# Performance work log

Hardware: AMD Instinct MI355X
Metric: run time of the kernel (lower is better)

Reference implementation:

```python
import jax, jax.numpy as jnp
import numpy as np

B, T, P = 256, 64, 10          # games, vote steps, players (cell_num)
E = 64                          # embedding_size -> node feat dim 2E=128
D = 2 * E
HID = 64                        # lstm_hidden_size
EPS = 1e-8


def setup_inputs() -> dict:
    key = jax.random.key(0)
    ks = jax.random.split(key, 12)
    s = 0.1  # param init scale
    return {
        "x": jax.random.normal(ks[0], (B, T, P, D), jnp.float32),
        "A_pos": jax.random.uniform(ks[1], (B, T, P, P), jnp.float32),
        "A_neg": jax.random.uniform(ks[2], (B, T, P, P), jnp.float32),
        "W_pos_base": s * jax.random.normal(ks[3], (2 * D, 32), jnp.float32),
        "b_pos_base": jnp.zeros((32,), jnp.float32),
        "W_neg_base": s * jax.random.normal(ks[4], (2 * D, 32), jnp.float32),
        "b_neg_base": jnp.zeros((32,), jnp.float32),
        "W_pos_deep": s * jax.random.normal(ks[5], (2, 7 * 32, 32), jnp.float32),
        "b_pos_deep": jnp.zeros((2, 32), jnp.float32),
        "W_neg_deep": s * jax.random.normal(ks[6], (2, 7 * 32, 32), jnp.float32),
        "b_neg_deep": jnp.zeros((2, 32), jnp.float32),
        "W_ih": s * jax.random.normal(ks[7], (P, 4 * HID, 2 * 32), jnp.float32),
        "W_hh": s * jax.random.normal(ks[8], (P, 4 * HID, HID), jnp.float32),
        "b_ih": jnp.zeros((P, 4 * HID), jnp.float32),
        "b_hh": jnp.zeros((P, 4 * HID), jnp.float32),
    }


def _sgcn(x, A_pos, A_neg, W_pos_base, b_pos_base, W_neg_base, b_neg_base,
          W_pos_deep, b_pos_deep, W_neg_deep, b_neg_deep):
    # mean aggregation: row-normalized signed adjacencies, shape [B,T,P,P]
    An_p = A_pos / (jnp.sum(A_pos, axis=-1, keepdims=True) + EPS)
    An_n = A_neg / (jnp.sum(A_neg, axis=-1, keepdims=True) + EPS)
    agg = lambda A, h: jnp.einsum('btij,btjd->btid', A, h)
    # base aggregators: cat([mean_neighbors, self]) @ W  -> [B,T,P,32]
    h_pos = jnp.tanh(jnp.concatenate([agg(An_p, x), x], -1) @ W_pos_base + b_pos_base)
    h_neg = jnp.tanh(jnp.concatenate([agg(An_n, x), x], -1) @ W_neg_base + b_neg_base)
    # two deep layers per sign: 7 concatenated 32-d blocks
    for i in range(2):
        ap_p, ap_n = agg(An_p, h_pos), agg(An_p, h_neg)
        an_p, an_n = agg(An_n, h_pos), agg(An_n, h_neg)
        common = [ap_p, ap_n, an_p, an_n, h_pos, h_neg]
        new_pos = jnp.tanh(jnp.concatenate(common + [h_pos], -1) @ W_pos_deep[i] + b_pos_deep[i])
        new_neg = jnp.tanh(jnp.concatenate(common + [h_neg], -1) @ W_neg_deep[i] + b_neg_deep[i])
        h_pos, h_neg = new_pos, new_neg
    return jnp.concatenate([h_pos, h_neg], -1)  # [B,T,P,64]


def _lstm(z, W_ih, W_hh, b_ih, b_hh):
    # per-player LSTMCell recurrence over vote steps (torch.nn.LSTMCell math)
    zT = jnp.moveaxis(z, 1, 0)  # [T,B,P,64]
    bias = b_ih + b_hh          # [P,4H]

    def step(carry, z_t):
        h, c = carry  # [B,P,H]
        gates = (jnp.einsum('bpi,pgi->bpg', z_t, W_ih)
                 + jnp.einsum('bph,pgh->bpg', h, W_hh) + bias)
        i, f, g, o = jnp.split(gates, 4, axis=-1)
        c_new = jax.nn.sigmoid(f) * c + jax.nn.sigmoid(i) * jnp.tanh(g)
        h_new = jax.nn.sigmoid(o) * jnp.tanh(c_new)
        return (h_new, c_new), h_new

    init = (jnp.zeros((z.shape[0], P, HID), z.dtype),
            jnp.zeros((z.shape[0], P, HID), z.dtype))
    _, hs = jax.lax.scan(step, init, zT)
    return jnp.moveaxis(hs, 0, 1)  # [B,T,P,H]


def reference(x, A_pos, A_neg, W_pos_base, b_pos_base, W_neg_base, b_neg_base,
              W_pos_deep, b_pos_deep, W_neg_deep, b_neg_deep,
              W_ih, W_hh, b_ih, b_hh):
    z = _sgcn(x, A_pos, A_neg, W_pos_base, b_pos_base, W_neg_base, b_neg_base,
              W_pos_deep, b_pos_deep, W_neg_deep, b_neg_deep)
    return _lstm(z, W_ih, W_hh, b_ih, b_hh)
```

## Files before the change

### kernel.cpp

```cpp
#include <hip/hip_runtime.h>
#include <stdint.h>

#define Bg 256
#define Tg 64
#define Pg 10
#define NG 8
#define GL 4

typedef _Float16 half2v __attribute__((ext_vector_type(2)));
typedef _Float16 f16x8 __attribute__((ext_vector_type(8)));
typedef float f32x4v __attribute__((ext_vector_type(4)));

__device__ __forceinline__ float dot2(uint32_t a, uint32_t b, float c) {
#if __has_builtin(__builtin_amdgcn_fdot2)
    return __builtin_amdgcn_fdot2(__builtin_bit_cast(half2v, a),
                                  __builtin_bit_cast(half2v, b), c, false);
#else
    float d;
    asm("v_dot2_f32_f16 %0, %1, %2, %3"
        : "=v"(d) : "v"(a), "v"(b), "v"(c));
    return d;
#endif
}

__device__ __forceinline__ uint32_t pkh2(float lo, float hi) {
    half2v h; h.x = (_Float16)lo; h.y = (_Float16)hi;
    return __builtin_bit_cast(uint32_t, h);
}
__device__ __forceinline__ uint16_t f2h(float f) {
    _Float16 h = (_Float16)f;
    return __builtin_bit_cast(uint16_t, h);
}
__device__ __forceinline__ float h2f(uint16_t u) {
    _Float16 h = __builtin_bit_cast(_Float16, u);
    return (float)h;
}
__device__ __forceinline__ float2 up2(uint32_t u) {
    half2v h = __builtin_bit_cast(half2v, u);
    return make_float2((float)h.x, (float)h.y);
}
__device__ __forceinline__ float sigmoidf_(float x) {
    return 1.0f / (1.0f + __expf(-x));
}
__device__ __forceinline__ float fast_tanh(float x) {
    float e = __expf(2.0f * x);
    return (e - 1.0f) / (e + 1.0f);
}

__global__ __launch_bounds__(512) void sgcn_kernel(
    const float* __restrict__ x,
    const float* __restrict__ A_pos,
    const float* __restrict__ A_neg,
    const float* __restrict__ Wpb,
    const float* __restrict__ bpb,
    const float* __restrict__ Wnb,
    const float* __restrict__ bnb,
    const float* __restrict__ Wpd,
    const float* __restrict__ bpd,
    const float* __restrict__ Wnd,
    const float* __restrict__ bnd,
    uint32_t* __restrict__ z)
{
    __shared__ __align__(16) uint32_t WLu[8192];
    __shared__ __align__(16) float As[NG][2][10][10];
    __shared__ float rsv[NG][2][10];
    __shared__ __align__(16) uint32_t Xsu[NG][10][64];
    __shared__ __align__(16) uint32_t H16a[NG][10][16][2];
    __shared__ __align__(16) uint32_t H16b[NG][10][16][2];

    const int tid = threadIdx.x;
    const int bt0 = blockIdx.x * NG;
    const int g = tid >> 6;
    const int s = (tid >> 5) & 1;
    const int k = tid & 31;

    for (int e = tid; e < 8192; e += 512) {
        int tb = e >> 12;
        int r = e & 4095;
        int d2g = r >> 8;
        int r2 = r & 255;
        int ln = r2 >> 2;
        int j  = r2 & 3;
        int ss = ln >> 5, kk = ln & 31;
        int d2 = d2g * 4 + j;
        const float* Ws = (ss ? Wnb : Wpb) + (tb * 128 + 2 * d2) * 32 + kk;
        WLu[e] = pkh2(Ws[0], Ws[32]);
    }
    for (int e = tid; e < NG * 640; e += 512) {
        int gg = e / 640, r = e - gg * 640;
        const float2* xp = reinterpret_cast<const float2*>(
            x + (size_t)(bt0 + gg) * 1280);
        float2 v = xp[r];
        (&Xsu[0][0][0])[e] = pkh2(v.x, v.y);
    }
    for (int e = tid; e < NG * 200; e += 512) {
        int gg = e / 200, r = e - gg * 200;
        int sg = r / 100, rr = r - sg * 100;
        (&As[gg][sg][0][0])[rr] =
            (sg ? A_neg : A_pos)[(size_t)(bt0 + gg) * 100 + rr];
    }
    __syncthreads();
    if (tid < NG * 20) {
        int gg = tid / 20, r = tid % 20, sg = r / 10, i = r % 10;
        float sum = 0.f;
        #pragma unroll
        for (int j = 0; j < 10; ++j) sum += As[gg][sg][i][j];
        rsv[gg][sg][i] = 1.0f / (sum + 1e-8f);
    }
    __syncthreads();
    for (int e = tid; e < NG * 200; e += 512) {
        int gg = e / 200, r = e - gg * 200;
        int sg = r / 100, rr = r - sg * 100;
        As[gg][sg][rr / 10][rr % 10] *= rsv[gg][sg][rr / 10];
    }
    __syncthreads();

    const int hslot = g * 640 + (k >> 1) * 4 + s * 2 + (k & 1);

    {
        float accY[10], accZ[10];
        #pragma unroll
        for (int i = 0; i < 10; ++i) { accY[i] = 0.f; accZ[i] = 0.f; }
        const uint32_t* Wt = &WLu[(s * 32 + k) * 4];
        const uint32_t* Xg = &Xsu[g][0][0];
        for (int d2g = 0; d2g < 16; ++d2g) {
            uint4 wt = *reinterpret_cast<const uint4*>(Wt + d2g * 256);
            uint4 wb = *reinterpret_cast<const uint4*>(Wt + 4096 + d2g * 256);
            #pragma unroll
            for (int i = 0; i < 10; ++i) {
                uint4 xv = *reinterpret_cast<const uint4*>(Xg + i * 64 + d2g * 4);
                accY[i] = dot2(xv.x, wt.x, accY[i]);
                accY[i] = dot2(xv.y, wt.y, accY[i]);
                accY[i] = dot2(xv.z, wt.z, accY[i]);
                accY[i] = dot2(xv.w, wt.w, accY[i]);
                accZ[i] = dot2(xv.x, wb.x, accZ[i]);
                accZ[i] = dot2(xv.y, wb.y, accZ[i]);
                accZ[i] = dot2(xv.z, wb.z, accZ[i]);
                accZ[i] = dot2(xv.w, wb.w, accZ[i]);
            }
        }
        float bb = (s ? bnb : bpb)[k];
        uint16_t* Hw = reinterpret_cast<uint16_t*>(&H16a[0][0][0][0]);
        const float2* Ar = reinterpret_cast<const float2*>(&As[g][s][0][0]);
        #pragma unroll
        for (int i = 0; i < 10; ++i) {
            float acc = accZ[i] + bb;
            #pragma unroll
            for (int m = 0; m < 5; ++m) {
                float2 a2 = Ar[i * 5 + m];
                acc += a2.x * accY[2 * m] + a2.y * accY[2 * m + 1];
            }
            Hw[hslot + i * 64] = f2h(fast_tanh(acc));
        }
    }
    __syncthreads();

    for (int l = 0; l < 2; ++l) {
        for (int e = tid; e < 6144; e += 512) {
            int blk = e >> 10;
            int r = e & 1023;
            int cpg = r >> 8;
            int r2 = r & 255;
            int ln = r2 >> 2;
            int j = r2 & 3;
            int ss = ln >> 5, kk = ln & 31;
            int cp = cpg * 4 + j;
            const float* Ws = (ss ? Wnd : Wpd) + l * 7168;
            int rk = blk * 32 + 2 * cp;
            float f0 = Ws[rk * 32 + kk];
            float f1 = Ws[(rk + 1) * 32 + kk];
            if (blk >= 4 && ((blk == 4) == (ss == 0))) {
                f0 += Ws[(192 + 2 * cp) * 32 + kk];
                f1 += Ws[(193 + 2 * cp) * 32 + kk];
            }
            WLu[e] = pkh2(f0, f1);
        }
        __syncthreads();

        const uint32_t* Hin = l ? &H16b[0][0][0][0] : &H16a[0][0][0][0];
        uint16_t* Hout16 = reinterpret_cast<uint16_t*>(
            l ? &H16a[0][0][0][0] : &H16b[0][0][0][0]);

        float U12[10], U34[10], Dd[10];
        #pragma unroll
        for (int i = 0; i < 10; ++i) { U12[i] = 0.f; U34[i] = 0.f; Dd[i] = 0.f; }
        const uint32_t* Wd = &WLu[(s * 32 + k) * 4];
        const uint32_t* Hg = Hin + g * 320;

        for (int cpg = 0; cpg < 4; ++cpg) {
            uint4 w0 = *reinterpret_cast<const uint4*>(Wd + 0 * 1024 + cpg * 256);
            uint4 w1 = *reinterpret_cast<const uint4*>(Wd + 1 * 1024 + cpg * 256);
            uint4 w2 = *reinterpret_cast<const uint4*>(Wd + 2 * 1024 + cpg * 256);
            uint4 w3 = *reinterpret_cast<const uint4*>(Wd + 3 * 1024 + cpg * 256);
            uint4 w4 = *reinterpret_cast<const uint4*>(Wd + 4 * 1024 + cpg * 256);
            uint4 w5 = *reinterpret_cast<const uint4*>(Wd + 5 * 1024 + cpg * 256);
            #pragma unroll
            for (int j = 0; j < 10; ++j) {
                uint4 ha = *reinterpret_cast<const uint4*>(Hg + j * 32 + cpg * 8);
                uint4 hb = *reinterpret_cast<const uint4*>(Hg + j * 32 + cpg * 8 + 4);
                U12[j] = dot2(ha.x, w0.x, U12[j]);
                U12[j] = dot2(ha.z, w0.y, U12[j]);
                U12[j] = dot2(hb.x, w0.z, U12[j]);
                U12[j] = dot2(hb.z, w0.w, U12[j]);
                U12[j] = dot2(ha.y, w1.x, U12[j]);
                U12[j] = dot2(ha.w, w1.y, U12[j]);
                U12[j] = dot2(hb.y, w1.z, U12[j]);
                U12[j] = dot2(hb.w, w1.w, U12[j]);
                U34[j] = dot2(ha.x, w2.x, U34[j]);
                U34[j] = dot2(ha.z, w2.y, U34[j]);
                U34[j] = dot2(hb.x, w2.z, U34[j]);
                U34[j] = dot2(hb.z, w2.w, U34[j]);
                U34[j] = dot2(ha.y, w3.x, U34[j]);
                U34[j] = dot2(ha.w, w3.y, U34[j]);
                U34[j] = dot2(hb.y, w3.z, U34[j]);
                U34[j] = dot2(hb.w, w3.w, U34[j]);
                Dd[j]  = dot2(ha.x, w4.x, Dd[j]);
                Dd[j]  = dot2(ha.z, w4.y, Dd[j]);
                Dd[j]  = dot2(hb.x, w4.z, Dd[j]);
                Dd[j]  = dot2(hb.z, w4.w, Dd[j]);
                Dd[j]  = dot2(ha.y, w5.x, Dd[j]);
                Dd[j]  = dot2(ha.w, w5.y, Dd[j]);
                Dd[j]  = dot2(hb.y, w5.z, Dd[j]);
                Dd[j]  = dot2(hb.w, w5.w, Dd[j]);
            }
        }
        float bb = (s ? bnd : bpd)[l * 32 + k];
        const float2* Ap = reinterpret_cast<const float2*>(&As[g][0][0][0]);
        const float2* An = reinterpret_cast<const float2*>(&As[g][1][0][0]);
        #pragma unroll
        for (int i = 0; i < 10; ++i) {
            float acc = Dd[i] + bb;
            #pragma unroll
            for (int m = 0; m < 5; ++m) {
                float2 ap = Ap[i * 5 + m], an = An[i * 5 + m];
                acc += ap.x * U12[2 * m] + ap.y * U12[2 * m + 1]
                     + an.x * U34[2 * m] + an.y * U34[2 * m + 1];
            }
            Hout16[hslot + i * 64] = f2h(fast_tanh(acc));
        }
        __syncthreads();
    }

    {
        uint32_t* zb = z + (size_t)bt0 * 320;
        const uint32_t* Hf = &H16a[0][0][0][0];
        for (int e = tid; e < NG * 320; e += 512) {
            int gg = e / 320, r = e - gg * 320;
            int i = r >> 5, m = r & 31;
            zb[e] = Hf[gg * 320 + i * 32 + (m & 15) * 2 + (m >> 4)];
        }
    }
}

__global__ __launch_bounds__(256) void lstm_kernel(
    const uint32_t* __restrict__ zin,
    const float* __restrict__ W_ih,
    const float* __restrict__ W_hh,
    const float* __restrict__ b_ih,
    const float* __restrict__ b_hh,
    float* __restrict__ out)
{
    __shared__ __align__(16) uint32_t Zb[2][4][64][4];
    __shared__ __align__(16) float gbuf[GL][264];

    const int tid = threadIdx.x;
    const int w   = tid >> 6;
    const int l   = tid & 63;
    const int lg  = l >> 4;
    const int ln_ = l & 15;
    const int p   = blockIdx.x % 10;
    const int b0  = (blockIdx.x / 10) * GL;

    f16x8 wfrag[16];
    #pragma unroll
    for (int tt = 0; tt < 4; ++tt) {
        int m = w * 64 + tt * 16 + ln_;
        #pragma unroll
        for (int kt = 0; kt < 4; ++kt) {
            const float* Wsrc = (kt < 2) ? W_ih : W_hh;
            const float* base = Wsrc + ((size_t)p * 256 + m) * 64 + (kt & 1) * 32 + lg * 8;
            float4 v0 = *reinterpret_cast<const float4*>(base);
            float4 v1 = *reinterpret_cast<const float4*>(base + 4);
            f16x8 a;
            a[0] = (_Float16)v0.x; a[1] = (_Float16)v0.y;
            a[2] = (_Float16)v0.z; a[3] = (_Float16)v0.w;
            a[4] = (_Float16)v1.x; a[5] = (_Float16)v1.y;
            a[6] = (_Float16)v1.z; a[7] = (_Float16)v1.w;
            wfrag[tt * 4 + kt] = a;
        }
    }
    f32x4v bias0, bias1, bias2, bias3;
    #pragma unroll
    for (int r = 0; r < 4; ++r) {
        int mb = w * 64 + lg * 4 + r;
        bias0[r] = b_ih[p * 256 + mb]      + b_hh[p * 256 + mb];
        bias1[r] = b_ih[p * 256 + mb + 16] + b_hh[p * 256 + mb + 16];
        bias2[r] = b_ih[p * 256 + mb + 32] + b_hh[p * 256 + mb + 32];
        bias3[r] = b_ih[p * 256 + mb + 48] + b_hh[p * 256 + mb + 48];
    }

    for (int e = tid; e < 2048; e += 256) (&Zb[0][0][0][0])[e] = 0u;
    const int sgm = (tid >> 5) & 3, sj = tid & 31;
    uint32_t znext = 0;
    if (tid >= 128) {
        uint32_t z0 = zin[((size_t)(b0 + sgm) * 64 + 0) * 320 + p * 32 + sj];
        Zb[0][sj >> 4][((sj >> 2) & 3) * 16 + sgm][sj & 3] = z0;
        znext = zin[((size_t)(b0 + sgm) * 64 + 1) * 320 + p * 32 + sj];
    }
    __syncthreads();

    const int agm = tid >> 5, ajh = tid & 31;
    float c0r = 0.f, c1r = 0.f;

    for (int t = 0; t < 64; ++t) {
        const int buf = t & 1;
        uint4 q0 = *reinterpret_cast<const uint4*>(&Zb[buf][0][l][0]);
        uint4 q1 = *reinterpret_cast<const uint4*>(&Zb[buf][1][l][0]);
        uint4 q2 = *reinterpret_cast<const uint4*>(&Zb[buf][2][l][0]);
        uint4 q3 = *reinterpret_cast<const uint4*>(&Zb[buf][3][l][0]);
        f16x8 bf0 = __builtin_bit_cast(f16x8, q0);
        f16x8 bf1 = __builtin_bit_cast(f16x8, q1);
        f16x8 bf2 = __builtin_bit_cast(f16x8, q2);
        f16x8 bf3 = __builtin_bit_cast(f16x8, q3);
        f32x4v a0 = bias0, a1 = bias1, a2 = bias2, a3 = bias3;
        a0 = __builtin_amdgcn_mfma_f32_16x16x32_f16(wfrag[0],  bf0, a0, 0, 0, 0);
        a0 = __builtin_amdgcn_mfma_f32_16x16x32_f16(wfrag[1],  bf1, a0, 0, 0, 0);
        a0 = __builtin_amdgcn_mfma_f32_16x16x32_f16(wfrag[2],  bf2, a0, 0, 0, 0);
        a0 = __builtin_amdgcn_mfma_f32_16x16x32_f16(wfrag[3],  bf3, a0, 0, 0, 0);
        a1 = __builtin_amdgcn_mfma_f32_16x16x32_f16(wfrag[4],  bf0, a1, 0, 0, 0);
        a1 = __builtin_amdgcn_mfma_f32_16x16x32_f16(wfrag[5],  bf1, a1, 0, 0, 0);
        a1 = __builtin_amdgcn_mfma_f32_16x16x32_f16(wfrag[6],  bf2, a1, 0, 0, 0);
        a1 = __builtin_amdgcn_mfma_f32_16x16x32_f16(wfrag[7],  bf3, a1, 0, 0, 0);
        a2 = __builtin_amdgcn_mfma_f32_16x16x32_f16(wfrag[8],  bf0, a2, 0, 0, 0);
        a2 = __builtin_amdgcn_mfma_f32_16x16x32_f16(wfrag[9],  bf1, a2, 0, 0, 0);
        a2 = __builtin_amdgcn_mfma_f32_16x16x32_f16(wfrag[10], bf2, a2, 0, 0, 0);
        a2 = __builtin_amdgcn_mfma_f32_16x16x32_f16(wfrag[11], bf3, a2, 0, 0, 0);
        a3 = __builtin_amdgcn_mfma_f32_16x16x32_f16(wfrag[12], bf0, a3, 0, 0, 0);
        a3 = __builtin_amdgcn_mfma_f32_16x16x32_f16(wfrag[13], bf1, a3, 0, 0, 0);
        a3 = __builtin_amdgcn_mfma_f32_16x16x32_f16(wfrag[14], bf2, a3, 0, 0, 0);
        a3 = __builtin_amdgcn_mfma_f32_16x16x32_f16(wfrag[15], bf3, a3, 0, 0, 0);
        if (ln_ < GL) {
            *reinterpret_cast<f32x4v*>(&gbuf[ln_][w * 64 +  0 + lg * 4]) = a0;
            *reinterpret_cast<f32x4v*>(&gbuf[ln_][w * 64 + 16 + lg * 4]) = a1;
            *reinterpret_cast<f32x4v*>(&gbuf[ln_][w * 64 + 32 + lg * 4]) = a2;
            *reinterpret_cast<f32x4v*>(&gbuf[ln_][w * 64 + 48 + lg * 4]) = a3;
        }
        __syncthreads();

        if (tid < 128) {
            float2 gi = *reinterpret_cast<const float2*>(&gbuf[agm][  0 + 2 * ajh]);
            float2 gf = *reinterpret_cast<const float2*>(&gbuf[agm][ 64 + 2 * ajh]);
            float2 gg = *reinterpret_cast<const float2*>(&gbuf[agm][128 + 2 * ajh]);
            float2 go = *reinterpret_cast<const float2*>(&gbuf[agm][192 + 2 * ajh]);
            float c0 = sigmoidf_(gf.x) * c0r + sigmoidf_(gi.x) * fast_tanh(gg.x);
            float c1 = sigmoidf_(gf.y) * c1r + sigmoidf_(gi.y) * fast_tanh(gg.y);
            float h0 = sigmoidf_(go.x) * fast_tanh(c0);
            float h1 = sigmoidf_(go.y) * fast_tanh(c1);
            c0r = c0; c1r = c1;
            int jp = 32 + ajh;
            Zb[buf ^ 1][jp >> 4][((jp >> 2) & 3) * 16 + agm][jp & 3] = pkh2(h0, h1);
            *reinterpret_cast<float2*>(
                &out[((size_t)(b0 + agm) * 64 + t) * 640 + p * 64 + 2 * ajh]) =
                make_float2(h0, h1);
        } else if (t < 63) {
            Zb[buf ^ 1][sj >> 4][((sj >> 2) & 3) * 16 + sgm][sj & 3] = znext;
            if (t < 62)
                znext = zin[((size_t)(b0 + sgm) * 64 + t + 2) * 320 + p * 32 + sj];
        }
        __syncthreads();
    }
}

extern "C" void kernel_launch(void* const* d_in, const int* in_sizes, int n_in,
                              void* d_out, int out_size, void* d_ws, size_t ws_size,
                              hipStream_t stream) {
    const float* x     = (const float*)d_in[0];
    const float* A_pos = (const float*)d_in[1];
    const float* A_neg = (const float*)d_in[2];
    const float* Wpb   = (const float*)d_in[3];
    const float* bpb   = (const float*)d_in[4];
    const float* Wnb   = (const float*)d_in[5];
    const float* bnb   = (const float*)d_in[6];
    const float* Wpd   = (const float*)d_in[7];
    const float* bpd   = (const float*)d_in[8];
    const float* Wnd   = (const float*)d_in[9];
    const float* bnd   = (const float*)d_in[10];
    const float* Wih   = (const float*)d_in[11];
    const float* Whh   = (const float*)d_in[12];
    const float* bih   = (const float*)d_in[13];
    const float* bhh   = (const float*)d_in[14];

    uint32_t* z = (uint32_t*)d_ws;
    float* out  = (float*)d_out;

    sgcn_kernel<<<(Bg * Tg) / NG, 512, 0, stream>>>(
        x, A_pos, A_neg, Wpb, bpb, Wnb, bnb, Wpd, bpd, Wnd, bnd, z);
    lstm_kernel<<<(Bg / GL) * Pg, 256, 0, stream>>>(
        z, Wih, Whh, bih, bhh, out);
}
```

Measured before the change: 468.2 us.

## Move SGCN dense projections onto MFMA tiles with reordered aggregation

New measurement: 387.4 us. 17.3% less time.

```diff
diff --git a/kernel.cpp b/kernel.cpp
--- a/kernel.cpp
+++ b/kernel.cpp
@@ -11,18 +11,6 @@
 typedef _Float16 f16x8 __attribute__((ext_vector_type(8)));
 typedef float f32x4v __attribute__((ext_vector_type(4)));
 
-__device__ __forceinline__ float dot2(uint32_t a, uint32_t b, float c) {
-#if __has_builtin(__builtin_amdgcn_fdot2)
-    return __builtin_amdgcn_fdot2(__builtin_bit_cast(half2v, a),
-                                  __builtin_bit_cast(half2v, b), c, false);
-#else
-    float d;
-    asm("v_dot2_f32_f16 %0, %1, %2, %3"
-        : "=v"(d) : "v"(a), "v"(b), "v"(c));
-    return d;
-#endif
-}
-
 __device__ __forceinline__ uint32_t pkh2(float lo, float hi) {
     half2v h; h.x = (_Float16)lo; h.y = (_Float16)hi;
     return __builtin_bit_cast(uint32_t, h);
@@ -35,16 +23,16 @@
     _Float16 h = __builtin_bit_cast(_Float16, u);
     return (float)h;
 }
-__device__ __forceinline__ float2 up2(uint32_t u) {
-    half2v h = __builtin_bit_cast(half2v, u);
-    return make_float2((float)h.x, (float)h.y);
-}
 __device__ __forceinline__ float sigmoidf_(float x) {
     return 1.0f / (1.0f + __expf(-x));
 }
 __device__ __forceinline__ float fast_tanh(float x) {
     float e = __expf(2.0f * x);
     return (e - 1.0f) / (e + 1.0f);
+}
+__device__ __forceinline__ f32x4v mfma16(uint4 a, uint4 b, f32x4v c) {
+    return __builtin_amdgcn_mfma_f32_16x16x32_f16(
+        __builtin_bit_cast(f16x8, a), __builtin_bit_cast(f16x8, b), c, 0, 0, 0);
 }
 
 __global__ __launch_bounds__(512) void sgcn_kernel(
@@ -61,194 +49,194 @@
     const float* __restrict__ bnd,
     uint32_t* __restrict__ z)
 {
-    __shared__ __align__(16) uint32_t WLu[8192];
-    __shared__ __align__(16) float As[NG][2][10][10];
-    __shared__ float rsv[NG][2][10];
-    __shared__ __align__(16) uint32_t Xsu[NG][10][64];
-    __shared__ __align__(16) uint32_t H16a[NG][10][16][2];
-    __shared__ __align__(16) uint32_t H16b[NG][10][16][2];
+    __shared__ __align__(16) uint32_t S[20240];
 
     const int tid = threadIdx.x;
     const int bt0 = blockIdx.x * NG;
-    const int g = tid >> 6;
-    const int s = (tid >> 5) & 1;
-    const int k = tid & 31;
-
+    const int wv = tid >> 6;
+    const int l  = tid & 63;
+    const int lg = l >> 4, ln = l & 15;
+    const int g = tid >> 6, s = (tid >> 5) & 1, k = tid & 31;
+
+    float* Asf  = reinterpret_cast<float*>(S);
+    float* rsvf = reinterpret_cast<float*>(S + 1600);
+    uint32_t* XF  = S + 1760;
+    uint32_t* HF  = S + 1760;
+    uint32_t* WFD = S + 4320;
+    uint32_t* WFB = S + 6880;
+    uint16_t* O2  = reinterpret_cast<uint16_t*>(S + 10464);
+    uint16_t* O1  = reinterpret_cast<uint16_t*>(S + 15072);
+    uint16_t* HFu = reinterpret_cast<uint16_t*>(S + 1760);
+    uint16_t* ZST = reinterpret_cast<uint16_t*>(S + 1760);
+
+    auto stageWFD = [&](int dl2) {
+        for (int e = tid; e < 6144; e += 512) {
+            int ep = e & 3, lane = (e >> 2) & 63, kt2 = (e >> 8) & 1, Nt = e >> 9;
+            int n = lane & 15, lgg = lane >> 4;
+            int kin = kt2 * 32 + lgg * 8 + ep * 2;
+            int c = Nt * 16 + n;
+            int s2 = c / 96, c2 = c - s2 * 96;
+            const float* Ws = (s2 ? Wnd : Wpd) + dl2 * 7168;
+            int bo = (c2 >> 5) * 2;
+            int col = c2 & 31;
+            float f0 = Ws[(bo * 32 + kin) * 32 + col];
+            float f1 = Ws[(bo * 32 + kin + 1) * 32 + col];
+            if (bo == 4 && ((s2 == 0) == (kin < 32))) {
+                int kh = kin & 31;
+                f0 += Ws[(192 + kh) * 32 + col];
+                f1 += Ws[(192 + kh + 1) * 32 + col];
+            }
+            WFD[e] = pkh2(f0, f1);
+        }
+    };
+
+    for (int e = tid; e < 5120; e += 512) {
+        int grow = e >> 6, dp = e & 63, d = dp << 1;
+        int gg = grow / 10, ii = grow - gg * 10;
+        float2 v = *reinterpret_cast<const float2*>(
+            x + (size_t)(bt0 + gg) * 1280 + ii * 128 + d);
+        int Mt = grow >> 4, lnn = grow & 15;
+        int kt = d >> 5, lgg = (d >> 3) & 3, ep = (d >> 1) & 3;
+        XF[((Mt * 4 + kt) * 64 + lgg * 16 + lnn) * 4 + ep] = pkh2(v.x, v.y);
+    }
     for (int e = tid; e < 8192; e += 512) {
-        int tb = e >> 12;
-        int r = e & 4095;
-        int d2g = r >> 8;
-        int r2 = r & 255;
-        int ln = r2 >> 2;
-        int j  = r2 & 3;
-        int ss = ln >> 5, kk = ln & 31;
-        int d2 = d2g * 4 + j;
-        const float* Ws = (ss ? Wnb : Wpb) + (tb * 128 + 2 * d2) * 32 + kk;
-        WLu[e] = pkh2(Ws[0], Ws[32]);
-    }
-    for (int e = tid; e < NG * 640; e += 512) {
-        int gg = e / 640, r = e - gg * 640;
-        const float2* xp = reinterpret_cast<const float2*>(
-            x + (size_t)(bt0 + gg) * 1280);
-        float2 v = xp[r];
-        (&Xsu[0][0][0])[e] = pkh2(v.x, v.y);
-    }
-    for (int e = tid; e < NG * 200; e += 512) {
+        int ep = e & 3, lane = (e >> 2) & 63, kt = (e >> 8) & 3, Nt = e >> 10;
+        int n = lane & 15, lgg = lane >> 4;
+        int kk2 = kt * 32 + lgg * 8 + ep * 2;
+        int c = Nt * 16 + n;
+        const float* Wsrc = (c & 64) ? Wnb : Wpb;
+        int cc = c & 63;
+        int rb = (cc & 32) ? 128 : 0;
+        int col = cc & 31;
+        WFB[e] = pkh2(Wsrc[(rb + kk2) * 32 + col], Wsrc[(rb + kk2 + 1) * 32 + col]);
+    }
+    for (int e = tid; e < 1600; e += 512) {
         int gg = e / 200, r = e - gg * 200;
         int sg = r / 100, rr = r - sg * 100;
-        (&As[gg][sg][0][0])[rr] =
+        Asf[(gg * 2 + sg) * 100 + rr] =
             (sg ? A_neg : A_pos)[(size_t)(bt0 + gg) * 100 + rr];
     }
     __syncthreads();
-    if (tid < NG * 20) {
+    if (tid < 160) {
         int gg = tid / 20, r = tid % 20, sg = r / 10, i = r % 10;
         float sum = 0.f;
         #pragma unroll
-        for (int j = 0; j < 10; ++j) sum += As[gg][sg][i][j];
-        rsv[gg][sg][i] = 1.0f / (sum + 1e-8f);
-    }
-    __syncthreads();
-    for (int e = tid; e < NG * 200; e += 512) {
+        for (int j = 0; j < 10; ++j) sum += Asf[(gg * 2 + sg) * 100 + i * 10 + j];
+        rsvf[(gg * 2 + sg) * 10 + i] = 1.0f / (sum + 1e-8f);
+    }
+    __syncthreads();
+    for (int e = tid; e < 1600; e += 512) {
         int gg = e / 200, r = e - gg * 200;
         int sg = r / 100, rr = r - sg * 100;
-        As[gg][sg][rr / 10][rr % 10] *= rsv[gg][sg][rr / 10];
-    }
-    __syncthreads();
-
-    const int hslot = g * 640 + (k >> 1) * 4 + s * 2 + (k & 1);
+        Asf[(gg * 2 + sg) * 100 + rr] *= rsvf[(gg * 2 + sg) * 10 + rr / 10];
+    }
+    __syncthreads();
 
     {
-        float accY[10], accZ[10];
-        #pragma unroll
-        for (int i = 0; i < 10; ++i) { accY[i] = 0.f; accZ[i] = 0.f; }
-        const uint32_t* Wt = &WLu[(s * 32 + k) * 4];
-        const uint32_t* Xg = &Xsu[g][0][0];
-        for (int d2g = 0; d2g < 16; ++d2g) {
-            uint4 wt = *reinterpret_cast<const uint4*>(Wt + d2g * 256);
-            uint4 wb = *reinterpret_cast<const uint4*>(Wt + 4096 + d2g * 256);
-            #pragma unroll
-            for (int i = 0; i < 10; ++i) {
-                uint4 xv = *reinterpret_cast<const uint4*>(Xg + i * 64 + d2g * 4);
-                accY[i] = dot2(xv.x, wt.x, accY[i]);
-                accY[i] = dot2(xv.y, wt.y, accY[i]);
-                accY[i] = dot2(xv.z, wt.z, accY[i]);
-                accY[i] = dot2(xv.w, wt.w, accY[i]);
-                accZ[i] = dot2(xv.x, wb.x, accZ[i]);
-                accZ[i] = dot2(xv.y, wb.y, accZ[i]);
-                accZ[i] = dot2(xv.z, wb.z, accZ[i]);
-                accZ[i] = dot2(xv.w, wb.w, accZ[i]);
-            }
-        }
+        uint4 b0 = *reinterpret_cast<const uint4*>(WFB + ((wv * 4 + 0) * 64 + l) * 4);
+        uint4 b1 = *reinterpret_cast<const uint4*>(WFB + ((wv * 4 + 1) * 64 + l) * 4);
+        uint4 b2 = *reinterpret_cast<const uint4*>(WFB + ((wv * 4 + 2) * 64 + l) * 4);
+        uint4 b3 = *reinterpret_cast<const uint4*>(WFB + ((wv * 4 + 3) * 64 + l) * 4);
+        #pragma unroll
+        for (int Mt = 0; Mt < 5; ++Mt) {
+            uint4 a0 = *reinterpret_cast<const uint4*>(XF + ((Mt * 4 + 0) * 64 + l) * 4);
+            uint4 a1 = *reinterpret_cast<const uint4*>(XF + ((Mt * 4 + 1) * 64 + l) * 4);
+            uint4 a2 = *reinterpret_cast<const uint4*>(XF + ((Mt * 4 + 2) * 64 + l) * 4);
+            uint4 a3 = *reinterpret_cast<const uint4*>(XF + ((Mt * 4 + 3) * 64 + l) * 4);
+            f32x4v c = {0.f, 0.f, 0.f, 0.f};
+            c = mfma16(a0, b0, c);
+            c = mfma16(a1, b1, c);
+            c = mfma16(a2, b2, c);
+            c = mfma16(a3, b3, c);
+            #pragma unroll
+            for (int r = 0; r < 4; ++r)
+                O1[(Mt * 16 + lg * 4 + r) * 128 + wv * 16 + ln] = f2h(c[r]);
+        }
+    }
+    __syncthreads();
+
+    stageWFD(0);
+    {
+        const float2* Ar = reinterpret_cast<const float2*>(Asf + (g * 2 + s) * 100);
+        float Yv[10];
+        #pragma unroll
+        for (int j = 0; j < 10; ++j)
+            Yv[j] = h2f(O1[(g * 10 + j) * 128 + s * 64 + k]);
         float bb = (s ? bnb : bpb)[k];
-        uint16_t* Hw = reinterpret_cast<uint16_t*>(&H16a[0][0][0][0]);
-        const float2* Ar = reinterpret_cast<const float2*>(&As[g][s][0][0]);
         #pragma unroll
         for (int i = 0; i < 10; ++i) {
-            float acc = accZ[i] + bb;
+            float acc = h2f(O1[(g * 10 + i) * 128 + s * 64 + 32 + k]) + bb;
             #pragma unroll
             for (int m = 0; m < 5; ++m) {
                 float2 a2 = Ar[i * 5 + m];
-                acc += a2.x * accY[2 * m] + a2.y * accY[2 * m + 1];
-            }
-            Hw[hslot + i * 64] = f2h(fast_tanh(acc));
-        }
-    }
-    __syncthreads();
-
-    for (int l = 0; l < 2; ++l) {
-        for (int e = tid; e < 6144; e += 512) {
-            int blk = e >> 10;
-            int r = e & 1023;
-            int cpg = r >> 8;
-            int r2 = r & 255;
-            int ln = r2 >> 2;
-            int j = r2 & 3;
-            int ss = ln >> 5, kk = ln & 31;
-            int cp = cpg * 4 + j;
-            const float* Ws = (ss ? Wnd : Wpd) + l * 7168;
-            int rk = blk * 32 + 2 * cp;
-            float f0 = Ws[rk * 32 + kk];
-            float f1 = Ws[(rk + 1) * 32 + kk];
-            if (blk >= 4 && ((blk == 4) == (ss == 0))) {
-                f0 += Ws[(192 + 2 * cp) * 32 + kk];
-                f1 += Ws[(193 + 2 * cp) * 32 + kk];
-            }
-            WLu[e] = pkh2(f0, f1);
+                acc += a2.x * Yv[2 * m] + a2.y * Yv[2 * m + 1];
+            }
+            int row = g * 10 + i;
+            HFu[(((row >> 4) * 2 + s) * 64 + ((k >> 3) & 3) * 16 + (row & 15)) * 8 + (k & 7)]
+                = f2h(fast_tanh(acc));
+        }
+    }
+    __syncthreads();
+
+    for (int dl = 0; dl < 2; ++dl) {
+        {
+            #pragma unroll
+            for (int pass = 0; pass < 2; ++pass) {
+                int Nt = wv + pass * 8;
+                if (pass == 1 && wv >= 4) break;
+                uint4 b0 = *reinterpret_cast<const uint4*>(WFD + ((Nt * 2 + 0) * 64 + l) * 4);
+                uint4 b1 = *reinterpret_cast<const uint4*>(WFD + ((Nt * 2 + 1) * 64 + l) * 4);
+                #pragma unroll
+                for (int Mt = 0; Mt < 5; ++Mt) {
+                    uint4 a0 = *reinterpret_cast<const uint4*>(HF + ((Mt * 2 + 0) * 64 + l) * 4);
+                    uint4 a1 = *reinterpret_cast<const uint4*>(HF + ((Mt * 2 + 1) * 64 + l) * 4);
+                    f32x4v c = {0.f, 0.f, 0.f, 0.f};
+                    c = mfma16(a0, b0, c);
+                    c = mfma16(a1, b1, c);
+                    #pragma unroll
+                    for (int r = 0; r < 4; ++r)
+                        O2[(Mt * 16 + lg * 4 + r) * 192 + Nt * 16 + ln] = f2h(c[r]);
+                }
+            }
         }
         __syncthreads();
 
-        const uint32_t* Hin = l ? &H16b[0][0][0][0] : &H16a[0][0][0][0];
-        uint16_t* Hout16 = reinterpret_cast<uint16_t*>(
-            l ? &H16a[0][0][0][0] : &H16b[0][0][0][0]);
-
-        float U12[10], U34[10], Dd[10];
-        #pragma unroll
-        for (int i = 0; i < 10; ++i) { U12[i] = 0.f; U34[i] = 0.f; Dd[i] = 0.f; }
-        const uint32_t* Wd = &WLu[(s * 32 + k) * 4];
-        const uint32_t* Hg = Hin + g * 320;
-
-        for (int cpg = 0; cpg < 4; ++cpg) {
-            uint4 w0 = *reinterpret_cast<const uint4*>(Wd + 0 * 1024 + cpg * 256);
-            uint4 w1 = *reinterpret_cast<const uint4*>(Wd + 1 * 1024 + cpg * 256);
-            uint4 w2 = *reinterpret_cast<const uint4*>(Wd + 2 * 1024 + cpg * 256);
-            uint4 w3 = *reinterpret_cast<const uint4*>(Wd + 3 * 1024 + cpg * 256);
-            uint4 w4 = *reinterpret_cast<const uint4*>(Wd + 4 * 1024 + cpg * 256);
-            uint4 w5 = *reinterpret_cast<const uint4*>(Wd + 5 * 1024 + cpg * 256);
+        if (dl == 0) stageWFD(1);
+        {
+            const float2* Ap = reinterpret_cast<const float2*>(Asf + g * 200);
+            const float2* An = reinterpret_cast<const float2*>(Asf + g * 200 + 100);
+            float U1[10], U3[10];
             #pragma unroll
             for (int j = 0; j < 10; ++j) {
-                uint4 ha = *reinterpret_cast<const uint4*>(Hg + j * 32 + cpg * 8);
-                uint4 hb = *reinterpret_cast<const uint4*>(Hg + j * 32 + cpg * 8 + 4);
-                U12[j] = dot2(ha.x, w0.x, U12[j]);
-                U12[j] = dot2(ha.z, w0.y, U12[j]);
-                U12[j] = dot2(hb.x, w0.z, U12[j]);
-                U12[j] = dot2(hb.z, w0.w, U12[j]);
-                U12[j] = dot2(ha.y, w1.x, U12[j]);
-                U12[j] = dot2(ha.w, w1.y, U12[j]);
-                U12[j] = dot2(hb.y, w1.z, U12[j]);
-                U12[j] = dot2(hb.w, w1.w, U12[j]);
-                U34[j] = dot2(ha.x, w2.x, U34[j]);
-                U34[j] = dot2(ha.z, w2.y, U34[j]);
-                U34[j] = dot2(hb.x, w2.z, U34[j]);
-                U34[j] = dot2(hb.z, w2.w, U34[j]);
-                U34[j] = dot2(ha.y, w3.x, U34[j]);
-                U34[j] = dot2(ha.w, w3.y, U34[j]);
-                U34[j] = dot2(hb.y, w3.z, U34[j]);
-                U34[j] = dot2(hb.w, w3.w, U34[j]);
-                Dd[j]  = dot2(ha.x, w4.x, Dd[j]);
-                Dd[j]  = dot2(ha.z, w4.y, Dd[j]);
-                Dd[j]  = dot2(hb.x, w4.z, Dd[j]);
-                Dd[j]  = dot2(hb.z, w4.w, Dd[j]);
-                Dd[j]  = dot2(ha.y, w5.x, Dd[j]);
-                Dd[j]  = dot2(ha.w, w5.y, Dd[j]);
-                Dd[j]  = dot2(hb.y, w5.z, Dd[j]);
-                Dd[j]  = dot2(hb.w, w5.w, Dd[j]);
-            }
-        }
-        float bb = (s ? bnd : bpd)[l * 32 + k];
-        const float2* Ap = reinterpret_cast<const float2*>(&As[g][0][0][0]);
-        const float2* An = reinterpret_cast<const float2*>(&As[g][1][0][0]);
-        #pragma unroll
-        for (int i = 0; i < 10; ++i) {
-            float acc = Dd[i] + bb;
-            #pragma unroll
-            for (int m = 0; m < 5; ++m) {
-                float2 ap = Ap[i * 5 + m], an = An[i * 5 + m];
-                acc += ap.x * U12[2 * m] + ap.y * U12[2 * m + 1]
-                     + an.x * U34[2 * m] + an.y * U34[2 * m + 1];
-            }
-            Hout16[hslot + i * 64] = f2h(fast_tanh(acc));
+                U1[j] = h2f(O2[(g * 10 + j) * 192 + s * 96 + k]);
+                U3[j] = h2f(O2[(g * 10 + j) * 192 + s * 96 + 32 + k]);
+            }
+            float bb = (s ? bnd : bpd)[dl * 32 + k];
+            #pragma unroll
+            for (int i = 0; i < 10; ++i) {
+                float acc = h2f(O2[(g * 10 + i) * 192 + s * 96 + 64 + k]) + bb;
+                #pragma unroll
+                for (int m = 0; m < 5; ++m) {
+                    float2 ap = Ap[i * 5 + m], an = An[i * 5 + m];
+                    acc += ap.x * U1[2 * m] + ap.y * U1[2 * m + 1]
+                         + an.x * U3[2 * m] + an.y * U3[2 * m + 1];
+                }
+                float hv = fast_tanh(acc);
+                int row = g * 10 + i;
+                if (dl == 0)
+                    HFu[(((row >> 4) * 2 + s) * 64 + ((k >> 3) & 3) * 16 + (row & 15)) * 8 + (k & 7)]
+                        = f2h(hv);
+                else
+                    ZST[row * 64 + s * 32 + k] = f2h(hv);
+            }
         }
         __syncthreads();
     }
 
     {
-        uint32_t* zb = z + (size_t)bt0 * 320;
-        const uint32_t* Hf = &H16a[0][0][0][0];
-        for (int e = tid; e < NG * 320; e += 512) {
-            int gg = e / 320, r = e - gg * 320;
-            int i = r >> 5, m = r & 31;
-            zb[e] = Hf[gg * 320 + i * 32 + (m & 15) * 2 + (m >> 4)];
-        }
+        const uint32_t* Zu = reinterpret_cast<const uint32_t*>(ZST);
+        for (int e = tid; e < 2560; e += 512)
+            z[(size_t)bt0 * 320 + e] = Zu[e];
     }
 }
 
```
